# Optimization experiments

Measured on AMD Instinct MI355X. Metric: run time of the kernel, lower is better.

## Reference

```python
import jax, jax.numpy as jnp
import numpy as np

B, T, E, H = 8, 1024, 128, 8
S = E // H  # 16, narrow per-head dim


def setup_inputs() -> dict:
    key = jax.random.key(0)
    ks = jax.random.split(key, 7)
    return {
        "x": jax.random.normal(ks[0], (B, T, E), dtype=jnp.float32),
        "masks": jax.random.randint(ks[1], (B, T), 0, 2, dtype=jnp.int32),
        "Wq": jax.random.normal(ks[2], (S, S), dtype=jnp.float32) * 0.05,
        "Wk": jax.random.normal(ks[3], (S, S), dtype=jnp.float32) * 0.05,
        "Wv": jax.random.normal(ks[4], (S, S), dtype=jnp.float32) * 0.05,
        "Wu": jax.random.normal(ks[5], (E, E), dtype=jnp.float32) * 0.05,
        "bu": jnp.zeros((E,), dtype=jnp.float32),
        "temporal_only": 1,
    }


def reference(x, masks, Wq, Wk, Wv, Wu, bu, temporal_only):
    b, t, e = x.shape
    h = H
    s = e // h
    x4 = x.reshape(b, t, h, s)
    # nn.Linear(s, s, bias=False): y = x @ W.T, applied per head
    q = jnp.einsum('bths,ds->bthd', x4, Wq)
    k = jnp.einsum('bths,ds->bthd', x4, Wk)
    v = jnp.einsum('bths,ds->bthd', x4, Wv)
    scale = jnp.float32(e) ** 0.25
    q = q / scale
    k = k / scale
    # (b, h, t, t) attention logits
    dot = jnp.einsum('bqhd,bkhd->bhqk', q, k)
    # temporal_only masking: masks is (b, t), applied on key axis then query axis
    m = masks.astype(bool)
    neg = jnp.float32(-1e9)
    dot = jnp.where(m[:, None, None, :], dot, neg)
    dot = jnp.where(m[:, None, :, None], dot, neg)
    attn = jax.nn.softmax(dot, axis=-1)
    # post-softmax zeroing with the same masks
    attn = jnp.where(m[:, None, None, :], attn, jnp.float32(0.0))
    attn = jnp.where(m[:, None, :, None], attn, jnp.float32(0.0))
    out = jnp.einsum('bhqk,bkhd->bqhd', attn, v).reshape(b, t, h * s)
    return out @ Wu.T + bu
```

## Files before the change

kernel.cpp:

```cpp
#include <hip/hip_runtime.h>

#define NB 8
#define NT 1024
#define NE 128
#define NH 8
#define NS 16

#define WS_Q 0
#define WS_K 1048576
#define WS_V 2097152
#define WS_Y 3145728
#define WS_VIDX 4194304

#define WT_PITCH 132

typedef float v2f __attribute__((ext_vector_type(2)));

static __device__ __forceinline__ v2f vlo(const float4 v) { return v2f{v.x, v.y}; }
static __device__ __forceinline__ v2f vhi(const float4 v) { return v2f{v.z, v.w}; }
static __device__ __forceinline__ v2f pfma(v2f a, v2f b, v2f c) {
  return __builtin_elementwise_fma(a, b, c);
}

static __device__ __forceinline__ void fma4(float4& acc, float s, const float4 v) {
  v2f lo = pfma(v2f{s, s}, vlo(v), vlo(acc));
  v2f hi = pfma(v2f{s, s}, vhi(v), vhi(acc));
  acc.x = lo.x; acc.y = lo.y; acc.z = hi.x; acc.w = hi.y;
}

static __device__ __forceinline__ float dot16p(const float4 q0, const float4 q1,
                                               const float4 q2, const float4 q3,
                                               const float4 k0, const float4 k1,
                                               const float4 k2, const float4 k3) {
  v2f a = vlo(q0) * vlo(k0);
  v2f b = vhi(q0) * vhi(k0);
  a = pfma(vlo(q1), vlo(k1), a);
  b = pfma(vhi(q1), vhi(k1), b);
  a = pfma(vlo(q2), vlo(k2), a);
  b = pfma(vhi(q2), vhi(k2), b);
  a = pfma(vlo(q3), vlo(k3), a);
  b = pfma(vhi(q3), vhi(k3), b);
  v2f c = a + b;
  return c.x + c.y;
}

__global__ __launch_bounds__(256) void qkv_kernel(
    const float* __restrict__ x, const int* __restrict__ masks,
    const float* __restrict__ Wq, const float* __restrict__ Wk,
    const float* __restrict__ Wv, float* __restrict__ Q, float* __restrict__ K,
    float* __restrict__ V, int* __restrict__ vidx, int* __restrict__ vcount) {
  if (blockIdx.x >= 1024) {
    const int b = blockIdx.x - 1024;
    const int lane = threadIdx.x;
    if (lane < 64) {
      int base = 0;
      for (int c = 0; c < NT; c += 64) {
        int t = c + lane;
        int v = masks[b * NT + t] != 0;
        unsigned long long bal = __ballot(v);
        int pos = base + __popcll(bal & ((1ull << lane) - 1ull));
        if (v) vidx[b * NT + pos] = t;
        base += __popcll(bal);
      }
      if (lane == 0) vcount[b] = base;
    }
    return;
  }
  __shared__ __align__(16) float xs[64 * 20];
  const int tid = threadIdx.x;
  const int h = blockIdx.x & 7;
  const int rg = blockIdx.x >> 3;
  const int b = rg >> 4;
  const int base = rg << 6;
  {
    const int sr = tid >> 2, sq = tid & 3;
    float4 xv = *(const float4*)(x + (size_t)(base + sr) * 128 + h * 16 + sq * 4);
    *(float4*)(xs + sr * 20 + sq * 4) = xv;
  }
  const int d = tid & 15;
  const int r = (tid >> 4) << 2;
  const float4* wq4 = (const float4*)(Wq + d * 16);
  const float4 wq0 = wq4[0], wq1 = wq4[1], wq2 = wq4[2], wq3 = wq4[3];
  const float4* wk4 = (const float4*)(Wk + d * 16);
  const float4 wk0 = wk4[0], wk1 = wk4[1], wk2 = wk4[2], wk3 = wk4[3];
  const float4* wv4 = (const float4*)(Wv + d * 16);
  const float4 wv0 = wv4[0], wv1 = wv4[1], wv2 = wv4[2], wv3 = wv4[3];
  const float invs = 0.08838834764831845f;
  __syncthreads();
#pragma unroll
  for (int i = 0; i < 4; i++) {
    const int row = r + i;
    const float4* xp = (const float4*)(xs + row * 20);
    const float4 x0 = xp[0], x1 = xp[1], x2 = xp[2], x3 = xp[3];
    float aq = dot16p(x0, x1, x2, x3, wq0, wq1, wq2, wq3);
    float ak = dot16p(x0, x1, x2, x3, wk0, wk1, wk2, wk3);
    float av = dot16p(x0, x1, x2, x3, wv0, wv1, wv2, wv3);
    const int t = (base + row) & 1023;
    size_t o = ((size_t)(b * NH + h) * NT + t) * NS + d;
    Q[o] = aq * invs;
    K[o] = ak;
    V[o] = av;
  }
}

__global__ __launch_bounds__(512) void attn_kernel(
    const float* __restrict__ Q, const float* __restrict__ K,
    const float* __restrict__ V, const int* __restrict__ vidx,
    const int* __restrict__ vcount, float* __restrict__ Y) {
  __shared__ __align__(16) float smem[10240];
  float* Ks = smem;
  float* Vs = smem + 2048;
  const int tid = threadIdx.x;
  const int lane = tid & 63;
  const int s = tid >> 6;
  const int bh = blockIdx.x & 63;
  const int tile = blockIdx.x >> 6;
  const int b = bh >> 3, h = bh & 7;
  const int tbase = tile << 8;
  const int nv = vcount[b];
  if (tbase >= nv) return;

  float4 q[4][4];
#pragma unroll
  for (int qq = 0; qq < 4; qq++) {
    int cq = tbase + (qq << 6) + lane;
    int cqc = (cq < nv) ? cq : (nv - 1);
    int tq = vidx[b * NT + cqc];
    const float4* qg = (const float4*)(Q + ((size_t)bh * NT + tq) * NS);
    q[qq][0] = qg[0]; q[qq][1] = qg[1]; q[qq][2] = qg[2]; q[qq][3] = qg[3];
  }
  v2f o[4][8];
  float m[4], l[4];
#pragma unroll
  for (int qq = 0; qq < 4; qq++) {
    m[qq] = -1e30f; l[qq] = 0.f;
#pragma unroll
    for (int k = 0; k < 8; k++) o[qq][k] = v2f{0.f, 0.f};
  }

  for (int k0 = 0; k0 < nv; k0 += 128) {
    __syncthreads();
    {
      const int quad = tid & 3;
      const int jr = tid >> 2;
      int j = k0 + jr;
      float4 kv = {0, 0, 0, 0}, vv = {0, 0, 0, 0};
      if (j < nv) {
        int kk = vidx[b * NT + j];
        size_t bse = ((size_t)bh * NT + kk) * NS + (quad << 2);
        kv = *(const float4*)(K + bse);
        vv = *(const float4*)(V + bse);
      }
      *(float4*)(Ks + jr * 16 + (quad << 2)) = kv;
      *(float4*)(Vs + jr * 16 + (quad << 2)) = vv;
    }
    __syncthreads();
    int jmax = nv - k0;
    if (jmax > 128) jmax = 128;
    for (int g = 0; g < 4; g++) {
      const int rb = s + (g << 5);
      if (rb >= jmax) break;
      float sc[4][4];
#pragma unroll
      for (int i = 0; i < 4; i++) {
        const float4* kr = (const float4*)(Ks + (rb + (i << 3)) * 16);
        const float4 k0v = kr[0], k1v = kr[1], k2v = kr[2], k3v = kr[3];
#pragma unroll
        for (int qq = 0; qq < 4; qq++)
          sc[qq][i] =
              dot16p(q[qq][0], q[qq][1], q[qq][2], q[qq][3], k0v, k1v, k2v, k3v);
      }
#pragma unroll
      for (int i = 0; i < 4; i++)
        if (rb + (i << 3) >= jmax) {
          sc[0][i] = -1e30f; sc[1][i] = -1e30f;
          sc[2][i] = -1e30f; sc[3][i] = -1e30f;
        }
      float p[4][4];
#pragma unroll
      for (int qq = 0; qq < 4; qq++) {
        float mb =
            fmaxf(fmaxf(sc[qq][0], sc[qq][1]), fmaxf(sc[qq][2], sc[qq][3]));
        if (mb > m[qq]) {
          float al = __expf(m[qq] - mb);
          v2f al2 = {al, al};
          l[qq] *= al;
#pragma unroll
          for (int k = 0; k < 8; k++) o[qq][k] *= al2;
          m[qq] = mb;
        }
        p[qq][0] = __expf(sc[qq][0] - m[qq]);
        p[qq][1] = __expf(sc[qq][1] - m[qq]);
        p[qq][2] = __expf(sc[qq][2] - m[qq]);
        p[qq][3] = __expf(sc[qq][3] - m[qq]);
        l[qq] += (p[qq][0] + p[qq][1]) + (p[qq][2] + p[qq][3]);
      }
#pragma unroll
      for (int i = 0; i < 4; i++) {
        const float4* vr = (const float4*)(Vs + (rb + (i << 3)) * 16);
        const float4 v0 = vr[0], v1 = vr[1], v2 = vr[2], v3 = vr[3];
#pragma unroll
        for (int qq = 0; qq < 4; qq++) {
          const v2f pq = {p[qq][i], p[qq][i]};
          o[qq][0] = pfma(pq, vlo(v0), o[qq][0]);
          o[qq][1] = pfma(pq, vhi(v0), o[qq][1]);
          o[qq][2] = pfma(pq, vlo(v1), o[qq][2]);
          o[qq][3] = pfma(pq, vhi(v1), o[qq][3]);
          o[qq][4] = pfma(pq, vlo(v2), o[qq][4]);
          o[qq][5] = pfma(pq, vhi(v2), o[qq][5]);
          o[qq][6] = pfma(pq, vlo(v3), o[qq][6]);
          o[qq][7] = pfma(pq, vhi(v3), o[qq][7]);
        }
      }
    }
  }

  float* om = smem;
#pragma unroll
  for (int ph = 0; ph < 4; ph++) {
    __syncthreads();
    {
      float* pa = om + (s * 64 + lane) * 20;
#pragma unroll
      for (int k = 0; k < 8; k++) *(v2f*)(pa + k * 2) = o[ph][k];
      pa[16] = m[ph];
      pa[17] = l[ph];
    }
    __syncthreads();
    {
      const int q8 = tid >> 3;
      const int sub = tid & 7;
      const int cq = tbase + (ph << 6) + q8;
      if (cq < nv) {
        float ms[8], ls[8];
#pragma unroll
        for (int ss = 0; ss < 8; ss++) {
          const float* pp = om + (ss * 64 + q8) * 20;
          ms[ss] = pp[16];
          ls[ss] = pp[17];
        }
        float M = fmaxf(fmaxf(fmaxf(ms[0], ms[1]), fmaxf(ms[2], ms[3])),
                        fmaxf(fmaxf(ms[4], ms[5]), fmaxf(ms[6], ms[7])));
        float L = 0.f;
        v2f y = {0.f, 0.f};
#pragma unroll
        for (int ss = 0; ss < 8; ss++) {
          float f = __expf(ms[ss] - M);
          L = fmaf(f, ls[ss], L);
          v2f ov = *(const v2f*)(om + (ss * 64 + q8) * 20 + sub * 2);
          y = pfma(v2f{f, f}, ov, y);
        }
        const int tq = vidx[b * NT + cq];
        const float inv = (L > 0.f) ? (1.0f / L) : 0.f;
        y *= v2f{inv, inv};
        *(v2f*)(Y + ((size_t)b * NT + tq) * NE + h * NS + sub * 2) = y;
      }
    }
  }
}

__global__ __launch_bounds__(256) void proj_kernel(
    const float* __restrict__ Y, const int* __restrict__ masks,
    const float* __restrict__ Wu, const float* __restrict__ bu,
    float* __restrict__ out) {
  __shared__ __align__(16) float Wt[64 * WT_PITCH];
  __shared__ __align__(16) float Yt[16 * 128];
  const int tid = threadIdx.x;
  const int r0 = blockIdx.x * 16;
  const float4* yg = (const float4*)(Y + (size_t)r0 * 128);
  float4* yt4 = (float4*)Yt;
  {
    const float4 z = {0, 0, 0, 0};
    const int m0 = masks[r0 + (tid >> 5)];
    const int m1 = masks[r0 + 8 + (tid >> 5)];
    float4 v0 = yg[tid];
    float4 v1 = yg[tid + 256];
    yt4[tid] = m0 ? v0 : z;
    yt4[tid + 256] = m1 ? v1 : z;
  }
  const int c0 = (tid & 31) << 2;
  const int rg = (tid >> 5) & 3;
  const int eh = tid >> 7;
  float4 acc0 = {0, 0, 0, 0}, acc1 = {0, 0, 0, 0}, acc2 = {0, 0, 0, 0},
         acc3 = {0, 0, 0, 0};
  for (int e0 = 0; e0 < 128; e0 += 64) {
    __syncthreads();
#pragma unroll
    for (int p = 0; p < 8; p++) {
      int idx = tid + p * 256;
      int c = idx >> 4;
      int es = (idx & 15) << 2;
      float4 w = *(const float4*)(Wu + c * 128 + e0 + es);
      Wt[(es + 0) * WT_PITCH + c] = w.x;
      Wt[(es + 1) * WT_PITCH + c] = w.y;
      Wt[(es + 2) * WT_PITCH + c] = w.z;
      Wt[(es + 3) * WT_PITCH + c] = w.w;
    }
    __syncthreads();
    const int eb = eh << 5;
    const float* y0 = Yt + (rg * 4 + 0) * 128 + e0 + eb;
    const float* y1 = Yt + (rg * 4 + 1) * 128 + e0 + eb;
    const float* y2 = Yt + (rg * 4 + 2) * 128 + e0 + eb;
    const float* y3 = Yt + (rg * 4 + 3) * 128 + e0 + eb;
#pragma unroll 4
    for (int e = 0; e < 32; e += 4) {
      const float* wb = Wt + (eb + e) * WT_PITCH + c0;
      float4 w0 = *(const float4*)(wb + 0 * WT_PITCH);
      float4 w1 = *(const float4*)(wb + 1 * WT_PITCH);
      float4 w2 = *(const float4*)(wb + 2 * WT_PITCH);
      float4 w3 = *(const float4*)(wb + 3 * WT_PITCH);
      float4 ya = *(const float4*)(y0 + e);
      float4 yb = *(const float4*)(y1 + e);
      float4 yc = *(const float4*)(y2 + e);
      float4 yd = *(const float4*)(y3 + e);
      fma4(acc0, ya.x, w0); fma4(acc0, ya.y, w1); fma4(acc0, ya.z, w2); fma4(acc0, ya.w, w3);
      fma4(acc1, yb.x, w0); fma4(acc1, yb.y, w1); fma4(acc1, yb.z, w2); fma4(acc1, yb.w, w3);
      fma4(acc2, yc.x, w0); fma4(acc2, yc.y, w1); fma4(acc2, yc.z, w2); fma4(acc2, yc.w, w3);
      fma4(acc3, yd.x, w0); fma4(acc3, yd.y, w1); fma4(acc3, yd.z, w2); fma4(acc3, yd.w, w3);
    }
  }
  __syncthreads();
  if (eh == 1) {
    float* p = Wt + (tid & 127) * 20;
    *(float4*)(p + 0) = acc0; *(float4*)(p + 4) = acc1;
    *(float4*)(p + 8) = acc2; *(float4*)(p + 12) = acc3;
  }
  __syncthreads();
  if (eh == 0) {
    const float* p = Wt + tid * 20;
    float4 b4 = *(const float4*)(bu + c0);
    float4 q0 = *(const float4*)(p + 0);
    float4 q1 = *(const float4*)(p + 4);
    float4 q2 = *(const float4*)(p + 8);
    float4 q3 = *(const float4*)(p + 12);
    acc0.x += q0.x + b4.x; acc0.y += q0.y + b4.y; acc0.z += q0.z + b4.z; acc0.w += q0.w + b4.w;
    acc1.x += q1.x + b4.x; acc1.y += q1.y + b4.y; acc1.z += q1.z + b4.z; acc1.w += q1.w + b4.w;
    acc2.x += q2.x + b4.x; acc2.y += q2.y + b4.y; acc2.z += q2.z + b4.z; acc2.w += q2.w + b4.w;
    acc3.x += q3.x + b4.x; acc3.y += q3.y + b4.y; acc3.z += q3.z + b4.z; acc3.w += q3.w + b4.w;
    *(float4*)(out + (size_t)(r0 + rg * 4 + 0) * 128 + c0) = acc0;
    *(float4*)(out + (size_t)(r0 + rg * 4 + 1) * 128 + c0) = acc1;
    *(float4*)(out + (size_t)(r0 + rg * 4 + 2) * 128 + c0) = acc2;
    *(float4*)(out + (size_t)(r0 + rg * 4 + 3) * 128 + c0) = acc3;
  }
}

extern "C" void kernel_launch(void* const* d_in, const int* in_sizes, int n_in,
                              void* d_out, int out_size, void* d_ws,
                              size_t ws_size, hipStream_t stream) {
  const float* x = (const float*)d_in[0];
  const int* masks = (const int*)d_in[1];
  const float* Wq = (const float*)d_in[2];
  const float* Wk = (const float*)d_in[3];
  const float* Wv = (const float*)d_in[4];
  const float* Wu = (const float*)d_in[5];
  const float* bu = (const float*)d_in[6];
  float* out = (float*)d_out;

  float* ws = (float*)d_ws;
  float* Q = ws + WS_Q;
  float* K = ws + WS_K;
  float* V = ws + WS_V;
  float* Y = ws + WS_Y;
  int* vidx = (int*)(ws + WS_VIDX);
  int* vcount = vidx + NB * NT;

  qkv_kernel<<<1024 + NB, 256, 0, stream>>>(x, masks, Wq, Wk, Wv, Q, K, V,
                                            vidx, vcount);
  attn_kernel<<<4 * NB * NH, 512, 0, stream>>>(Q, K, V, vidx, vcount, Y);
  proj_kernel<<<NB * NT / 16, 256, 0, stream>>>(Y, masks, Wu, bu, out);
}
```

Measured before the change: 135.6 us.

## Halve attention query tile to double grid size and peel partial key tile

```diff
diff --git a/kernel.cpp b/kernel.cpp
--- a/kernel.cpp
+++ b/kernel.cpp
@@ -116,71 +116,56 @@
   const int bh = blockIdx.x & 63;
   const int tile = blockIdx.x >> 6;
   const int b = bh >> 3, h = bh & 7;
-  const int tbase = tile << 8;
+  const int tbase = tile << 7;
   const int nv = vcount[b];
   if (tbase >= nv) return;
 
-  float4 q[4][4];
-#pragma unroll
-  for (int qq = 0; qq < 4; qq++) {
+  float4 q[2][4];
+#pragma unroll
+  for (int qq = 0; qq < 2; qq++) {
     int cq = tbase + (qq << 6) + lane;
     int cqc = (cq < nv) ? cq : (nv - 1);
     int tq = vidx[b * NT + cqc];
     const float4* qg = (const float4*)(Q + ((size_t)bh * NT + tq) * NS);
     q[qq][0] = qg[0]; q[qq][1] = qg[1]; q[qq][2] = qg[2]; q[qq][3] = qg[3];
   }
-  v2f o[4][8];
-  float m[4], l[4];
-#pragma unroll
-  for (int qq = 0; qq < 4; qq++) {
+  v2f o[2][8];
+  float m[2], l[2];
+#pragma unroll
+  for (int qq = 0; qq < 2; qq++) {
     m[qq] = -1e30f; l[qq] = 0.f;
 #pragma unroll
     for (int k = 0; k < 8; k++) o[qq][k] = v2f{0.f, 0.f};
   }
 
-  for (int k0 = 0; k0 < nv; k0 += 128) {
+  const int quad = tid & 3;
+  const int jr = tid >> 2;
+  const int nfull = nv & ~127;
+
+  for (int k0 = 0; k0 < nfull; k0 += 128) {
     __syncthreads();
     {
-      const int quad = tid & 3;
-      const int jr = tid >> 2;
-      int j = k0 + jr;
-      float4 kv = {0, 0, 0, 0}, vv = {0, 0, 0, 0};
-      if (j < nv) {
-        int kk = vidx[b * NT + j];
-        size_t bse = ((size_t)bh * NT + kk) * NS + (quad << 2);
-        kv = *(const float4*)(K + bse);
-        vv = *(const float4*)(V + bse);
-      }
-      *(float4*)(Ks + jr * 16 + (quad << 2)) = kv;
-      *(float4*)(Vs + jr * 16 + (quad << 2)) = vv;
-    }
-    __syncthreads();
-    int jmax = nv - k0;
-    if (jmax > 128) jmax = 128;
+      int kk = vidx[b * NT + k0 + jr];
+      size_t bse = ((size_t)bh * NT + kk) * NS + (quad << 2);
+      *(float4*)(Ks + jr * 16 + (quad << 2)) = *(const float4*)(K + bse);
+      *(float4*)(Vs + jr * 16 + (quad << 2)) = *(const float4*)(V + bse);
+    }
+    __syncthreads();
+#pragma unroll 1
     for (int g = 0; g < 4; g++) {
       const int rb = s + (g << 5);
-      if (rb >= jmax) break;
-      float sc[4][4];
+      float sc[2][4];
 #pragma unroll
       for (int i = 0; i < 4; i++) {
         const float4* kr = (const float4*)(Ks + (rb + (i << 3)) * 16);
         const float4 k0v = kr[0], k1v = kr[1], k2v = kr[2], k3v = kr[3];
-#pragma unroll
-        for (int qq = 0; qq < 4; qq++)
-          sc[qq][i] =
-              dot16p(q[qq][0], q[qq][1], q[qq][2], q[qq][3], k0v, k1v, k2v, k3v);
-      }
-#pragma unroll
-      for (int i = 0; i < 4; i++)
-        if (rb + (i << 3) >= jmax) {
-          sc[0][i] = -1e30f; sc[1][i] = -1e30f;
-          sc[2][i] = -1e30f; sc[3][i] = -1e30f;
-        }
-      float p[4][4];
-#pragma unroll
-      for (int qq = 0; qq < 4; qq++) {
-        float mb =
-            fmaxf(fmaxf(sc[qq][0], sc[qq][1]), fmaxf(sc[qq][2], sc[qq][3]));
+        sc[0][i] = dot16p(q[0][0], q[0][1], q[0][2], q[0][3], k0v, k1v, k2v, k3v);
+        sc[1][i] = dot16p(q[1][0], q[1][1], q[1][2], q[1][3], k0v, k1v, k2v, k3v);
+      }
+      float p[2][4];
+#pragma unroll
+      for (int qq = 0; qq < 2; qq++) {
+        float mb = fmaxf(fmaxf(sc[qq][0], sc[qq][1]), fmaxf(sc[qq][2], sc[qq][3]));
         if (mb > m[qq]) {
           float al = __expf(m[qq] - mb);
           v2f al2 = {al, al};
@@ -200,7 +185,7 @@
         const float4* vr = (const float4*)(Vs + (rb + (i << 3)) * 16);
         const float4 v0 = vr[0], v1 = vr[1], v2 = vr[2], v3 = vr[3];
 #pragma unroll
-        for (int qq = 0; qq < 4; qq++) {
+        for (int qq = 0; qq < 2; qq++) {
           const v2f pq = {p[qq][i], p[qq][i]};
           o[qq][0] = pfma(pq, vlo(v0), o[qq][0]);
           o[qq][1] = pfma(pq, vhi(v0), o[qq][1]);
@@ -215,9 +200,78 @@
     }
   }
 
+  if (nfull < nv) {
+    const int jmax = nv - nfull;
+    __syncthreads();
+    {
+      int j = nfull + jr;
+      float4 kv = {0, 0, 0, 0}, vv = {0, 0, 0, 0};
+      if (j < nv) {
+        int kk = vidx[b * NT + j];
+        size_t bse = ((size_t)bh * NT + kk) * NS + (quad << 2);
+        kv = *(const float4*)(K + bse);
+        vv = *(const float4*)(V + bse);
+      }
+      *(float4*)(Ks + jr * 16 + (quad << 2)) = kv;
+      *(float4*)(Vs + jr * 16 + (quad << 2)) = vv;
+    }
+    __syncthreads();
+#pragma unroll 1
+    for (int g = 0; g < 4; g++) {
+      const int rb = s + (g << 5);
+      if (rb >= jmax) break;
+      float sc[2][4];
+#pragma unroll
+      for (int i = 0; i < 4; i++) {
+        const float4* kr = (const float4*)(Ks + (rb + (i << 3)) * 16);
+        const float4 k0v = kr[0], k1v = kr[1], k2v = kr[2], k3v = kr[3];
+        sc[0][i] = dot16p(q[0][0], q[0][1], q[0][2], q[0][3], k0v, k1v, k2v, k3v);
+        sc[1][i] = dot16p(q[1][0], q[1][1], q[1][2], q[1][3], k0v, k1v, k2v, k3v);
+      }
+#pragma unroll
+      for (int i = 0; i < 4; i++)
+        if (rb + (i << 3) >= jmax) { sc[0][i] = -1e30f; sc[1][i] = -1e30f; }
+      float p[2][4];
+#pragma unroll
+      for (int qq = 0; qq < 2; qq++) {
+        float mb = fmaxf(fmaxf(sc[qq][0], sc[qq][1]), fmaxf(sc[qq][2], sc[qq][3]));
+        if (mb > m[qq]) {
+          float al = __expf(m[qq] - mb);
+          v2f al2 = {al, al};
+          l[qq] *= al;
+#pragma unroll
+          for (int k = 0; k < 8; k++) o[qq][k] *= al2;
+          m[qq] = mb;
+        }
+        p[qq][0] = __expf(sc[qq][0] - m[qq]);
+        p[qq][1] = __expf(sc[qq][1] - m[qq]);
+        p[qq][2] = __expf(sc[qq][2] - m[qq]);
+        p[qq][3] = __expf(sc[qq][3] - m[qq]);
+        l[qq] += (p[qq][0] + p[qq][1]) + (p[qq][2] + p[qq][3]);
+      }
+#pragma unroll
+      for (int i = 0; i < 4; i++) {
+        const float4* vr = (const float4*)(Vs + (rb + (i << 3)) * 16);
+        const float4 v0 = vr[0], v1 = vr[1], v2 = vr[2], v3 = vr[3];
+#pragma unroll
+        for (int qq = 0; qq < 2; qq++) {
+          const v2f pq = {p[qq][i], p[qq][i]};
+          o[qq][0] = pfma(pq, vlo(v0), o[qq][0]);
+          o[qq][1] = pfma(pq, vhi(v0), o[qq][1]);
+          o[qq][2] = pfma(pq, vlo(v1), o[qq][2]);
+          o[qq][3] = pfma(pq, vhi(v1), o[qq][3]);
+          o[qq][4] = pfma(pq, vlo(v2), o[qq][4]);
+          o[qq][5] = pfma(pq, vhi(v2), o[qq][5]);
+          o[qq][6] = pfma(pq, vlo(v3), o[qq][6]);
+          o[qq][7] = pfma(pq, vhi(v3), o[qq][7]);
+        }
+      }
+    }
+  }
+
   float* om = smem;
 #pragma unroll
-  for (int ph = 0; ph < 4; ph++) {
+  for (int ph = 0; ph < 2; ph++) {
     __syncthreads();
     {
       float* pa = om + (s * 64 + lane) * 20;
@@ -366,6 +420,6 @@
 
   qkv_kernel<<<1024 + NB, 256, 0, stream>>>(x, masks, Wq, Wk, Wv, Q, K, V,
                                             vidx, vcount);
-  attn_kernel<<<4 * NB * NH, 512, 0, stream>>>(Q, K, V, vidx, vcount, Y);
+  attn_kernel<<<8 * NB * NH, 512, 0, stream>>>(Q, K, V, vidx, vcount, Y);
   proj_kernel<<<NB * NT / 16, 256, 0, stream>>>(Y, masks, Wu, bu, out);
 }
```

New measurement: 138.4 us. +2.1%, slower.

## Compact K/V in QKV kernel and stream keys per query thread

Applied to the files above, without the earlier changes.

```diff
diff --git a/kernel.cpp b/kernel.cpp
--- a/kernel.cpp
+++ b/kernel.cpp
@@ -7,10 +7,10 @@
 #define NS 16
 
 #define WS_Q 0
-#define WS_K 1048576
-#define WS_V 2097152
+#define WS_KC 1048576
+#define WS_VC 2097152
 #define WS_Y 3145728
-#define WS_VIDX 4194304
+#define WS_VCNT 4194304
 
 #define WT_PITCH 132
 
@@ -26,6 +26,10 @@
   v2f lo = pfma(v2f{s, s}, vlo(v), vlo(acc));
   v2f hi = pfma(v2f{s, s}, vhi(v), vhi(acc));
   acc.x = lo.x; acc.y = lo.y; acc.z = hi.x; acc.w = hi.y;
+}
+
+static __device__ __forceinline__ void mul4(float4& a, float s) {
+  a.x *= s; a.y *= s; a.z *= s; a.w *= s;
 }
 
 static __device__ __forceinline__ float dot16p(const float4 q0, const float4 q1,
@@ -47,35 +51,29 @@
 __global__ __launch_bounds__(256) void qkv_kernel(
     const float* __restrict__ x, const int* __restrict__ masks,
     const float* __restrict__ Wq, const float* __restrict__ Wk,
-    const float* __restrict__ Wv, float* __restrict__ Q, float* __restrict__ K,
-    float* __restrict__ V, int* __restrict__ vidx, int* __restrict__ vcount) {
-  if (blockIdx.x >= 1024) {
-    const int b = blockIdx.x - 1024;
-    const int lane = threadIdx.x;
-    if (lane < 64) {
-      int base = 0;
-      for (int c = 0; c < NT; c += 64) {
-        int t = c + lane;
-        int v = masks[b * NT + t] != 0;
-        unsigned long long bal = __ballot(v);
-        int pos = base + __popcll(bal & ((1ull << lane) - 1ull));
-        if (v) vidx[b * NT + pos] = t;
-        base += __popcll(bal);
-      }
-      if (lane == 0) vcount[b] = base;
-    }
-    return;
-  }
+    const float* __restrict__ Wv, float* __restrict__ Q,
+    float* __restrict__ Kc, float* __restrict__ Vc, int* __restrict__ vcount) {
   __shared__ __align__(16) float xs[64 * 20];
+  __shared__ int posl[64];
   const int tid = threadIdx.x;
   const int h = blockIdx.x & 7;
   const int rg = blockIdx.x >> 3;
   const int b = rg >> 4;
-  const int base = rg << 6;
+  const int bt = (rg & 15) << 6;
   {
     const int sr = tid >> 2, sq = tid & 3;
-    float4 xv = *(const float4*)(x + (size_t)(base + sr) * 128 + h * 16 + sq * 4);
+    float4 xv =
+        *(const float4*)(x + (size_t)(b * NT + bt + sr) * 128 + h * 16 + sq * 4);
     *(float4*)(xs + sr * 20 + sq * 4) = xv;
+  }
+  if (tid < 64) {
+    int cnt = 0;
+    for (int c = 0; c < bt; c += 64)
+      cnt += __popcll(__ballot(masks[b * NT + c + tid] != 0));
+    int v = masks[b * NT + bt + tid] != 0;
+    unsigned long long bal = __ballot(v);
+    posl[tid] = v ? (cnt + __popcll(bal & ((1ull << tid) - 1ull))) : -1;
+    if (bt == NT - 64 && tid == 0) vcount[b] = cnt + __popcll(bal);
   }
   const int d = tid & 15;
   const int r = (tid >> 4) << 2;
@@ -95,168 +93,87 @@
     float aq = dot16p(x0, x1, x2, x3, wq0, wq1, wq2, wq3);
     float ak = dot16p(x0, x1, x2, x3, wk0, wk1, wk2, wk3);
     float av = dot16p(x0, x1, x2, x3, wv0, wv1, wv2, wv3);
-    const int t = (base + row) & 1023;
-    size_t o = ((size_t)(b * NH + h) * NT + t) * NS + d;
-    Q[o] = aq * invs;
-    K[o] = ak;
-    V[o] = av;
-  }
-}
-
-__global__ __launch_bounds__(512) void attn_kernel(
-    const float* __restrict__ Q, const float* __restrict__ K,
-    const float* __restrict__ V, const int* __restrict__ vidx,
+    const int t = bt + row;
+    Q[((size_t)(b * NH + h) * NT + t) * NS + d] = aq * invs;
+    const int pp = posl[row];
+    if (pp >= 0) {
+      size_t oc = ((size_t)(b * NH + h) * NT + pp) * NS + d;
+      Kc[oc] = ak;
+      Vc[oc] = av;
+    }
+  }
+}
+
+__global__ __launch_bounds__(256) void attn_kernel(
+    const float* __restrict__ Q, const float* __restrict__ Kc,
+    const float* __restrict__ Vc, const int* __restrict__ masks,
     const int* __restrict__ vcount, float* __restrict__ Y) {
-  __shared__ __align__(16) float smem[10240];
-  float* Ks = smem;
-  float* Vs = smem + 2048;
   const int tid = threadIdx.x;
   const int lane = tid & 63;
-  const int s = tid >> 6;
+  const int w = tid >> 6;
   const int bh = blockIdx.x & 63;
-  const int tile = blockIdx.x >> 6;
+  const int qg = blockIdx.x >> 6;
   const int b = bh >> 3, h = bh & 7;
-  const int tbase = tile << 8;
+  const int t0 = ((qg << 2) + w) * 64 + lane;
   const int nv = vcount[b];
-  if (tbase >= nv) return;
-
-  float4 q[4][4];
-#pragma unroll
-  for (int qq = 0; qq < 4; qq++) {
-    int cq = tbase + (qq << 6) + lane;
-    int cqc = (cq < nv) ? cq : (nv - 1);
-    int tq = vidx[b * NT + cqc];
-    const float4* qg = (const float4*)(Q + ((size_t)bh * NT + tq) * NS);
-    q[qq][0] = qg[0]; q[qq][1] = qg[1]; q[qq][2] = qg[2]; q[qq][3] = qg[3];
-  }
-  v2f o[4][8];
-  float m[4], l[4];
-#pragma unroll
-  for (int qq = 0; qq < 4; qq++) {
-    m[qq] = -1e30f; l[qq] = 0.f;
-#pragma unroll
-    for (int k = 0; k < 8; k++) o[qq][k] = v2f{0.f, 0.f};
-  }
-
-  for (int k0 = 0; k0 < nv; k0 += 128) {
-    __syncthreads();
+  const float* Kb = Kc + (size_t)bh * NT * NS;
+  const float* Vb = Vc + (size_t)bh * NT * NS;
+  const float4* qp = (const float4*)(Q + ((size_t)bh * NT + t0) * NS);
+  const float4 q0 = qp[0], q1 = qp[1], q2 = qp[2], q3 = qp[3];
+  float m = -1e30f, l = 0.f;
+  float4 o0 = {0, 0, 0, 0}, o1 = {0, 0, 0, 0}, o2 = {0, 0, 0, 0},
+         o3 = {0, 0, 0, 0};
+
+#define KEYSTEP(K0, K1, K2, K3, V0, V1, V2, V3)            \
+  do {                                                     \
+    float s = dot16p(q0, q1, q2, q3, K0, K1, K2, K3);      \
+    if (s > m) {                                           \
+      float al = __expf(m - s);                            \
+      l *= al;                                             \
+      mul4(o0, al); mul4(o1, al); mul4(o2, al); mul4(o3, al); \
+      m = s;                                               \
+    }                                                      \
+    float p = __expf(s - m);                               \
+    l += p;                                                \
+    fma4(o0, p, V0); fma4(o1, p, V1);                      \
+    fma4(o2, p, V2); fma4(o3, p, V3);                      \
+  } while (0)
+
+  float4 ka0, ka1, ka2, ka3, va0, va1, va2, va3;
+  float4 kb0, kb1, kb2, kb3, vb0, vb1, vb2, vb3;
+  int j = 0;
+  if (nv > 0) {
+    const float4* kp = (const float4*)Kb;
+    ka0 = kp[0]; ka1 = kp[1]; ka2 = kp[2]; ka3 = kp[3];
+    const float4* vp = (const float4*)Vb;
+    va0 = vp[0]; va1 = vp[1]; va2 = vp[2]; va3 = vp[3];
+  }
+  for (; j + 2 <= nv; j += 2) {
     {
-      const int quad = tid & 3;
-      const int jr = tid >> 2;
-      int j = k0 + jr;
-      float4 kv = {0, 0, 0, 0}, vv = {0, 0, 0, 0};
-      if (j < nv) {
-        int kk = vidx[b * NT + j];
-        size_t bse = ((size_t)bh * NT + kk) * NS + (quad << 2);
-        kv = *(const float4*)(K + bse);
-        vv = *(const float4*)(V + bse);
-      }
-      *(float4*)(Ks + jr * 16 + (quad << 2)) = kv;
-      *(float4*)(Vs + jr * 16 + (quad << 2)) = vv;
-    }
-    __syncthreads();
-    int jmax = nv - k0;
-    if (jmax > 128) jmax = 128;
-    for (int g = 0; g < 4; g++) {
-      const int rb = s + (g << 5);
-      if (rb >= jmax) break;
-      float sc[4][4];
-#pragma unroll
-      for (int i = 0; i < 4; i++) {
-        const float4* kr = (const float4*)(Ks + (rb + (i << 3)) * 16);
-        const float4 k0v = kr[0], k1v = kr[1], k2v = kr[2], k3v = kr[3];
-#pragma unroll
-        for (int qq = 0; qq < 4; qq++)
-          sc[qq][i] =
-              dot16p(q[qq][0], q[qq][1], q[qq][2], q[qq][3], k0v, k1v, k2v, k3v);
-      }
-#pragma unroll
-      for (int i = 0; i < 4; i++)
-        if (rb + (i << 3) >= jmax) {
-          sc[0][i] = -1e30f; sc[1][i] = -1e30f;
-          sc[2][i] = -1e30f; sc[3][i] = -1e30f;
-        }
-      float p[4][4];
-#pragma unroll
-      for (int qq = 0; qq < 4; qq++) {
-        float mb =
-            fmaxf(fmaxf(sc[qq][0], sc[qq][1]), fmaxf(sc[qq][2], sc[qq][3]));
-        if (mb > m[qq]) {
-          float al = __expf(m[qq] - mb);
-          v2f al2 = {al, al};
-          l[qq] *= al;
-#pragma unroll
-          for (int k = 0; k < 8; k++) o[qq][k] *= al2;
-          m[qq] = mb;
-        }
-        p[qq][0] = __expf(sc[qq][0] - m[qq]);
-        p[qq][1] = __expf(sc[qq][1] - m[qq]);
-        p[qq][2] = __expf(sc[qq][2] - m[qq]);
-        p[qq][3] = __expf(sc[qq][3] - m[qq]);
-        l[qq] += (p[qq][0] + p[qq][1]) + (p[qq][2] + p[qq][3]);
-      }
-#pragma unroll
-      for (int i = 0; i < 4; i++) {
-        const float4* vr = (const float4*)(Vs + (rb + (i << 3)) * 16);
-        const float4 v0 = vr[0], v1 = vr[1], v2 = vr[2], v3 = vr[3];
-#pragma unroll
-        for (int qq = 0; qq < 4; qq++) {
-          const v2f pq = {p[qq][i], p[qq][i]};
-          o[qq][0] = pfma(pq, vlo(v0), o[qq][0]);
-          o[qq][1] = pfma(pq, vhi(v0), o[qq][1]);
-          o[qq][2] = pfma(pq, vlo(v1), o[qq][2]);
-          o[qq][3] = pfma(pq, vhi(v1), o[qq][3]);
-          o[qq][4] = pfma(pq, vlo(v2), o[qq][4]);
-          o[qq][5] = pfma(pq, vhi(v2), o[qq][5]);
-          o[qq][6] = pfma(pq, vlo(v3), o[qq][6]);
-          o[qq][7] = pfma(pq, vhi(v3), o[qq][7]);
-        }
-      }
-    }
-  }
-
-  float* om = smem;
-#pragma unroll
-  for (int ph = 0; ph < 4; ph++) {
-    __syncthreads();
+      const float4* kp = (const float4*)(Kb + (size_t)(j + 1) * NS);
+      kb0 = kp[0]; kb1 = kp[1]; kb2 = kp[2]; kb3 = kp[3];
+      const float4* vp = (const float4*)(Vb + (size_t)(j + 1) * NS);
+      vb0 = vp[0]; vb1 = vp[1]; vb2 = vp[2]; vb3 = vp[3];
+    }
+    KEYSTEP(ka0, ka1, ka2, ka3, va0, va1, va2, va3);
     {
-      float* pa = om + (s * 64 + lane) * 20;
-#pragma unroll
-      for (int k = 0; k < 8; k++) *(v2f*)(pa + k * 2) = o[ph][k];
-      pa[16] = m[ph];
-      pa[17] = l[ph];
-    }
-    __syncthreads();
-    {
-      const int q8 = tid >> 3;
-      const int sub = tid & 7;
-      const int cq = tbase + (ph << 6) + q8;
-      if (cq < nv) {
-        float ms[8], ls[8];
-#pragma unroll
-        for (int ss = 0; ss < 8; ss++) {
-          const float* pp = om + (ss * 64 + q8) * 20;
-          ms[ss] = pp[16];
-          ls[ss] = pp[17];
-        }
-        float M = fmaxf(fmaxf(fmaxf(ms[0], ms[1]), fmaxf(ms[2], ms[3])),
-                        fmaxf(fmaxf(ms[4], ms[5]), fmaxf(ms[6], ms[7])));
-        float L = 0.f;
-        v2f y = {0.f, 0.f};
-#pragma unroll
-        for (int ss = 0; ss < 8; ss++) {
-          float f = __expf(ms[ss] - M);
-          L = fmaf(f, ls[ss], L);
-          v2f ov = *(const v2f*)(om + (ss * 64 + q8) * 20 + sub * 2);
-          y = pfma(v2f{f, f}, ov, y);
-        }
-        const int tq = vidx[b * NT + cq];
-        const float inv = (L > 0.f) ? (1.0f / L) : 0.f;
-        y *= v2f{inv, inv};
-        *(v2f*)(Y + ((size_t)b * NT + tq) * NE + h * NS + sub * 2) = y;
-      }
-    }
-  }
+      const float4* kp = (const float4*)(Kb + (size_t)(j + 2) * NS);
+      ka0 = kp[0]; ka1 = kp[1]; ka2 = kp[2]; ka3 = kp[3];
+      const float4* vp = (const float4*)(Vb + (size_t)(j + 2) * NS);
+      va0 = vp[0]; va1 = vp[1]; va2 = vp[2]; va3 = vp[3];
+    }
+    KEYSTEP(kb0, kb1, kb2, kb3, vb0, vb1, vb2, vb3);
+  }
+  if (j < nv) {
+    KEYSTEP(ka0, ka1, ka2, ka3, va0, va1, va2, va3);
+  }
+#undef KEYSTEP
+
+  const int qm = masks[b * NT + t0];
+  const float inv = (qm != 0 && l > 0.f) ? (1.0f / l) : 0.f;
+  mul4(o0, inv); mul4(o1, inv); mul4(o2, inv); mul4(o3, inv);
+  float4* yo = (float4*)(Y + ((size_t)b * NT + t0) * NE + h * NS);
+  yo[0] = o0; yo[1] = o1; yo[2] = o2; yo[3] = o3;
 }
 
 __global__ __launch_bounds__(256) void proj_kernel(
@@ -358,14 +275,13 @@
 
   float* ws = (float*)d_ws;
   float* Q = ws + WS_Q;
-  float* K = ws + WS_K;
-  float* V = ws + WS_V;
+  float* Kc = ws + WS_KC;
+  float* Vc = ws + WS_VC;
   float* Y = ws + WS_Y;
-  int* vidx = (int*)(ws + WS_VIDX);
-  int* vcount = vidx + NB * NT;
-
-  qkv_kernel<<<1024 + NB, 256, 0, stream>>>(x, masks, Wq, Wk, Wv, Q, K, V,
-                                            vidx, vcount);
-  attn_kernel<<<4 * NB * NH, 512, 0, stream>>>(Q, K, V, vidx, vcount, Y);
+  int* vcount = (int*)(ws + WS_VCNT);
+
+  qkv_kernel<<<1024, 256, 0, stream>>>(x, masks, Wq, Wk, Wv, Q, Kc, Vc,
+                                       vcount);
+  attn_kernel<<<4 * NB * NH, 256, 0, stream>>>(Q, Kc, Vc, masks, vcount, Y);
   proj_kernel<<<NB * NT / 16, 256, 0, stream>>>(Y, masks, Wu, bu, out);
 }
```

Result: slower. 236.4 us (+74.3%).
